# Optimization experiments

Measured on AMD Instinct MI355X. Metric: run time of the kernel, lower is better.

The kernel has to match this reference:

```python
import jax, jax.numpy as jnp
import numpy as np

ALPHA = 0.4
STEPS = 4
EPSILON = 0.005

N_NODES = 4096
N_EDGES = 131072
D_FEAT = 128


def setup_inputs() -> dict:
    key = jax.random.key(0)
    k1, k2, k3, k4 = jax.random.split(key, 4)
    x = jax.random.normal(k1, (N_NODES, D_FEAT), dtype=jnp.float32)
    src = jax.random.randint(k2, (N_EDGES,), 0, N_NODES)
    dst = jax.random.randint(k3, (N_EDGES,), 0, N_NODES)
    edge_index = jnp.stack([src, dst], axis=0).astype(jnp.int64)
    edge_attr = jax.random.uniform(k4, (N_EDGES,), dtype=jnp.float32)
    return {"x": x, "edge_index": edge_index, "edge_attr": edge_attr}


def reference(x, edge_index, edge_attr):
    # PPR power series: result = sum_i theta_i * A_i, where
    #   A_0 = edge pattern with unit values, A_1 = A (edge_attr),
    #   A_{i+1} = threshold_eps(A @ A_i).
    # Dense [N,N] representation: thresholding (dropping entries < eps in the
    # sparse original) is exactly zeroing those entries here; jit-compatible
    # since sparse nnz is data-dependent.
    N = x.shape[0]
    src, dst = edge_index[0], edge_index[1]
    A = jnp.zeros((N, N), dtype=edge_attr.dtype).at[src, dst].add(edge_attr)
    P0 = jnp.zeros((N, N), dtype=edge_attr.dtype).at[src, dst].add(1.0)

    mats = [P0, A]
    for _ in range(1, STEPS - 1):
        M = A @ mats[-1]
        M = jnp.where(M >= EPSILON, M, jnp.zeros((), dtype=M.dtype))
        mats.append(M)

    thetas = [ALPHA * (1.0 - ALPHA) ** i for i in range(STEPS)]
    out = thetas[0] * mats[0]
    for t, m in zip(thetas[1:], mats[1:]):
        out = out + t * m
    return out
```

## Files before the change

### kernel.cpp

```cpp
#include <hip/hip_runtime.h>

#define N_NODES 4096
#define EPS 0.005f
#define TH0 0.4f
#define TH1 0.24f
#define TH2 0.144f
#define TH3 0.0864f
#define JTILE 512
#define NTILES (N_NODES / JTILE)
#define RCAP 80
#define CPAD 16

typedef float v4f __attribute__((ext_vector_type(4)));
typedef unsigned int u32x4 __attribute__((ext_vector_type(4)));


static __device__ __forceinline__ float lo16(unsigned int u) {
    return __uint_as_float(u << 16);
}
static __device__ __forceinline__ float hi16(unsigned int u) {
    return __uint_as_float(u & 0xffff0000u);
}

static __device__ __forceinline__ unsigned short f2bf(float f) {
    union { float f; unsigned int i; } x;
    x.f = f;
    unsigned int r = x.i + 0x7fff + ((x.i >> 16) & 1u);
    return (unsigned short)(r >> 16);
}

__global__ void scatter_kernel(const int* __restrict__ idx,
                               const float* __restrict__ attr, int E,
                               int* __restrict__ counts, int2* __restrict__ pairs) {
    int e = blockIdx.x * blockDim.x + threadIdx.x;
    if (e < E) {
        int s = idx[e];
        int d = idx[e + E];
        float a = attr[e];
        int pos = atomicAdd(&counts[s * CPAD], 1);
        if (pos < RCAP) pairs[s * RCAP + pos] = make_int2(d, __float_as_int(a));
    }
}

__global__ __launch_bounds__(256)
void m2_kernel(const int* __restrict__ counts, const int2* __restrict__ pairs,
               unsigned short* __restrict__ m2) {
    __shared__ float acc[N_NODES];
    __shared__ int   kcol[RCAP];
    __shared__ float kval[RCAP];
    __shared__ int   kcnt[RCAP];
    int i = blockIdx.x;
    int t = threadIdx.x;
    float4 z = make_float4(0.f, 0.f, 0.f, 0.f);
    for (int j4 = t; j4 < N_NODES / 4; j4 += 256) ((float4*)acc)[j4] = z;
    int cnt = min(counts[i * CPAD], RCAP);
    if (t < cnt) {
        int2 p = pairs[i * RCAP + t];
        kcol[t] = p.x;
        kval[t] = __int_as_float(p.y);
        kcnt[t] = min(counts[p.x * CPAD], RCAP);
    }
    __syncthreads();
    int gid = t >> 3, gl = t & 7;
    for (int q = gid; q < cnt; q += 32) {
        float a = kval[q];
        int fb = kcol[q] * RCAP;
        int fn = kcnt[q];
        for (int f = gl; f < fn; f += 8) {
            int2 p = pairs[fb + f];
            unsafeAtomicAdd(&acc[p.x], a * __int_as_float(p.y));
        }
    }
    __syncthreads();
    size_t rb = (size_t)i * N_NODES;
    for (int j4 = t; j4 < N_NODES / 4; j4 += 256) {
        float4 v = ((const float4*)acc)[j4];
        ushort4 r;
        r.x = (v.x >= EPS) ? f2bf(v.x) : (unsigned short)0;
        r.y = (v.y >= EPS) ? f2bf(v.y) : (unsigned short)0;
        r.z = (v.z >= EPS) ? f2bf(v.z) : (unsigned short)0;
        r.w = (v.w >= EPS) ? f2bf(v.w) : (unsigned short)0;
        ((ushort4*)(m2 + rb))[j4] = r;
    }
}

__global__ __launch_bounds__(128)
void out_kernel(const int* __restrict__ counts, const int2* __restrict__ pairs,
                const unsigned short* __restrict__ m2,
                float* __restrict__ out) {
    __shared__ float ap[2][JTILE];
    int lin = blockIdx.x;
    int tile = lin & 7;
    int jb = tile * JTILE;
    int t = threadIdx.x;
    int w = t >> 6, lane = t & 63;
    int i = 2 * (lin >> 3) + w;
    float* apw = ap[w];
    ((float4*)apw)[lane] = make_float4(0.f, 0.f, 0.f, 0.f);
    ((float4*)apw)[64 + lane] = make_float4(0.f, 0.f, 0.f, 0.f);
    int cnt = min(counts[i * CPAD], RCAP);
    const int2* pi = pairs + i * RCAP;
    for (int e = lane; e < cnt; e += 64) {
        int2 p = pi[e];
        int cl = p.x - jb;
        if ((unsigned)cl < (unsigned)JTILE)
            unsafeAtomicAdd(&apw[cl], TH0 + TH1 * __int_as_float(p.y));
    }
    int cnt8 = (cnt + 7) & ~7;
    const unsigned short* m2l = m2 + jb + 8 * lane;
    v4f acc0 = 0.f, acc1 = 0.f;
    for (int e = 0; e < cnt8; e += 8) {
        int4 q01 = *(const int4*)(pi + e);
        int4 q23 = *(const int4*)(pi + e + 2);
        int4 q45 = *(const int4*)(pi + e + 4);
        int4 q67 = *(const int4*)(pi + e + 6);
        int k0 = __builtin_amdgcn_readfirstlane(q01.x);
        int k1 = __builtin_amdgcn_readfirstlane(q01.z);
        int k2 = __builtin_amdgcn_readfirstlane(q23.x);
        int k3 = __builtin_amdgcn_readfirstlane(q23.z);
        int k4 = __builtin_amdgcn_readfirstlane(q45.x);
        int k5 = __builtin_amdgcn_readfirstlane(q45.z);
        int k6 = __builtin_amdgcn_readfirstlane(q67.x);
        int k7 = __builtin_amdgcn_readfirstlane(q67.z);
        float a0 = __int_as_float(q01.y), a1 = __int_as_float(q01.w);
        float a2 = __int_as_float(q23.y), a3 = __int_as_float(q23.w);
        float a4 = __int_as_float(q45.y), a5 = __int_as_float(q45.w);
        float a6 = __int_as_float(q67.y), a7 = __int_as_float(q67.w);
        u32x4 u0 = *(const u32x4*)(m2l + (size_t)k0 * N_NODES);
        u32x4 u1 = *(const u32x4*)(m2l + (size_t)k1 * N_NODES);
        u32x4 u2 = *(const u32x4*)(m2l + (size_t)k2 * N_NODES);
        u32x4 u3 = *(const u32x4*)(m2l + (size_t)k3 * N_NODES);
        u32x4 u4 = *(const u32x4*)(m2l + (size_t)k4 * N_NODES);
        u32x4 u5 = *(const u32x4*)(m2l + (size_t)k5 * N_NODES);
        u32x4 u6 = *(const u32x4*)(m2l + (size_t)k6 * N_NODES);
        u32x4 u7 = *(const u32x4*)(m2l + (size_t)k7 * N_NODES);
#define ACC8(uu, aa)                                \
        acc0.x = fmaf(aa, lo16(uu.x), acc0.x);      \
        acc0.y = fmaf(aa, hi16(uu.x), acc0.y);      \
        acc0.z = fmaf(aa, lo16(uu.y), acc0.z);      \
        acc0.w = fmaf(aa, hi16(uu.y), acc0.w);      \
        acc1.x = fmaf(aa, lo16(uu.z), acc1.x);      \
        acc1.y = fmaf(aa, hi16(uu.z), acc1.y);      \
        acc1.z = fmaf(aa, lo16(uu.w), acc1.z);      \
        acc1.w = fmaf(aa, hi16(uu.w), acc1.w);
        ACC8(u0, a0) ACC8(u1, a1) ACC8(u2, a2) ACC8(u3, a3)
        ACC8(u4, a4) ACC8(u5, a5) ACC8(u6, a6) ACC8(u7, a7)
#undef ACC8
    }
    u32x4 um = *(const u32x4*)(m2 + (size_t)i * N_NODES + jb + 8 * lane);
    float4 p0 = ((const float4*)apw)[2 * lane];
    float4 p1 = ((const float4*)apw)[2 * lane + 1];
    v4f r0, r1;
    r0.x = p0.x + TH2 * lo16(um.x) + TH3 * ((acc0.x >= EPS) ? acc0.x : 0.0f);
    r0.y = p0.y + TH2 * hi16(um.x) + TH3 * ((acc0.y >= EPS) ? acc0.y : 0.0f);
    r0.z = p0.z + TH2 * lo16(um.y) + TH3 * ((acc0.z >= EPS) ? acc0.z : 0.0f);
    r0.w = p0.w + TH2 * hi16(um.y) + TH3 * ((acc0.w >= EPS) ? acc0.w : 0.0f);
    r1.x = p1.x + TH2 * lo16(um.z) + TH3 * ((acc1.x >= EPS) ? acc1.x : 0.0f);
    r1.y = p1.y + TH2 * hi16(um.z) + TH3 * ((acc1.y >= EPS) ? acc1.y : 0.0f);
    r1.z = p1.z + TH2 * lo16(um.w) + TH3 * ((acc1.z >= EPS) ? acc1.z : 0.0f);
    r1.w = p1.w + TH2 * hi16(um.w) + TH3 * ((acc1.w >= EPS) ? acc1.w : 0.0f);
    float* o = out + (size_t)i * N_NODES + jb + 8 * lane;
    __builtin_nontemporal_store(r0, (v4f*)o);
    __builtin_nontemporal_store(r1, (v4f*)(o + 4));
}

extern "C" void kernel_launch(void* const* d_in, const int* in_sizes, int n_in,
                              void* d_out, int out_size, void* d_ws, size_t ws_size,
                              hipStream_t stream) {
    const int* idx = (const int*)d_in[1];
    const float* attr = (const float*)d_in[2];
    int E = in_sizes[1] / 2;

    char* ws = (char*)d_ws;
    int*  counts = (int*)(ws);
    int2* pairs  = (int2*)(ws + (256 << 10));
    unsigned short* m2 = (unsigned short*)(ws + (4 << 20));
    float* out   = (float*)d_out;

    (void)hipMemsetAsync(ws, 0,
                         (256 << 10) + N_NODES * RCAP * sizeof(int2), stream);
    scatter_kernel<<<(E + 255) / 256, 256, 0, stream>>>(idx, attr, E, counts, pairs);
    m2_kernel<<<N_NODES, 256, 0, stream>>>(counts, pairs, m2);
    out_kernel<<<(N_NODES / 2) * NTILES, 128, 0, stream>>>(counts, pairs, m2, out);
}
```

Before: 179.3 us.

## Software-pipeline gather loads in out_kernel and unroll m2 atomic scatter loop

Restructures the out_kernel neighbor loop into a double-buffered pipeline. The next batch of eight m2 row loads is issued before the current batch is consumed, and pair indices are prefetched two batches ahead. The diagonal m2 load is hoisted to the start and launch bounds now request 3 blocks per SM. In m2_kernel each lane issues four pair loads before its atomics, giving more memory-level parallelism. The costs are much higher register pressure, which could force spills under the tighter launch bound, and more complex loop control.

```diff
diff --git a/kernel.cpp b/kernel.cpp
--- a/kernel.cpp
+++ b/kernel.cpp
@@ -62,13 +62,21 @@
     }
     __syncthreads();
     int gid = t >> 3, gl = t & 7;
+    int2 zp = make_int2(0, 0);
     for (int q = gid; q < cnt; q += 32) {
         float a = kval[q];
         int fb = kcol[q] * RCAP;
         int fn = kcnt[q];
-        for (int f = gl; f < fn; f += 8) {
-            int2 p = pairs[fb + f];
-            unsafeAtomicAdd(&acc[p.x], a * __int_as_float(p.y));
+        for (int f0 = gl; f0 < fn; f0 += 32) {
+            int i1 = f0 + 8, i2 = f0 + 16, i3 = f0 + 24;
+            int2 p0 = pairs[fb + f0];
+            int2 p1 = (i1 < fn) ? pairs[fb + i1] : zp;
+            int2 p2 = (i2 < fn) ? pairs[fb + i2] : zp;
+            int2 p3 = (i3 < fn) ? pairs[fb + i3] : zp;
+            unsafeAtomicAdd(&acc[p0.x], a * __int_as_float(p0.y));
+            unsafeAtomicAdd(&acc[p1.x], a * __int_as_float(p1.y));
+            unsafeAtomicAdd(&acc[p2.x], a * __int_as_float(p2.y));
+            unsafeAtomicAdd(&acc[p3.x], a * __int_as_float(p3.y));
         }
     }
     __syncthreads();
@@ -84,7 +92,41 @@
     }
 }
 
-__global__ __launch_bounds__(128)
+#define ACC8(uu, aa)                                \
+        acc0.x = fmaf(aa, lo16(uu.x), acc0.x);      \
+        acc0.y = fmaf(aa, hi16(uu.x), acc0.y);      \
+        acc0.z = fmaf(aa, lo16(uu.y), acc0.z);      \
+        acc0.w = fmaf(aa, hi16(uu.y), acc0.w);      \
+        acc1.x = fmaf(aa, lo16(uu.z), acc1.x);      \
+        acc1.y = fmaf(aa, hi16(uu.z), acc1.y);      \
+        acc1.z = fmaf(aa, lo16(uu.w), acc1.z);      \
+        acc1.w = fmaf(aa, hi16(uu.w), acc1.w);
+
+#define EXTR(E0_, E1_, E2_, E3_, K, A)                                              \
+        K##0 = __builtin_amdgcn_readfirstlane(E0_.x); A##0 = __int_as_float(E0_.y); \
+        K##1 = __builtin_amdgcn_readfirstlane(E0_.z); A##1 = __int_as_float(E0_.w); \
+        K##2 = __builtin_amdgcn_readfirstlane(E1_.x); A##2 = __int_as_float(E1_.y); \
+        K##3 = __builtin_amdgcn_readfirstlane(E1_.z); A##3 = __int_as_float(E1_.w); \
+        K##4 = __builtin_amdgcn_readfirstlane(E2_.x); A##4 = __int_as_float(E2_.y); \
+        K##5 = __builtin_amdgcn_readfirstlane(E2_.z); A##5 = __int_as_float(E2_.w); \
+        K##6 = __builtin_amdgcn_readfirstlane(E3_.x); A##6 = __int_as_float(E3_.y); \
+        K##7 = __builtin_amdgcn_readfirstlane(E3_.z); A##7 = __int_as_float(E3_.w);
+
+#define ISSUE8(K, U)                                                    \
+        U##0 = *(const u32x4*)(m2l + (size_t)K##0 * N_NODES);           \
+        U##1 = *(const u32x4*)(m2l + (size_t)K##1 * N_NODES);           \
+        U##2 = *(const u32x4*)(m2l + (size_t)K##2 * N_NODES);           \
+        U##3 = *(const u32x4*)(m2l + (size_t)K##3 * N_NODES);           \
+        U##4 = *(const u32x4*)(m2l + (size_t)K##4 * N_NODES);           \
+        U##5 = *(const u32x4*)(m2l + (size_t)K##5 * N_NODES);           \
+        U##6 = *(const u32x4*)(m2l + (size_t)K##6 * N_NODES);           \
+        U##7 = *(const u32x4*)(m2l + (size_t)K##7 * N_NODES);
+
+#define CONSUME8(U, A)                                                      \
+        ACC8(U##0, A##0) ACC8(U##1, A##1) ACC8(U##2, A##2) ACC8(U##3, A##3) \
+        ACC8(U##4, A##4) ACC8(U##5, A##5) ACC8(U##6, A##6) ACC8(U##7, A##7)
+
+__global__ __launch_bounds__(128, 3)
 void out_kernel(const int* __restrict__ counts, const int2* __restrict__ pairs,
                 const unsigned short* __restrict__ m2,
                 float* __restrict__ out) {
@@ -96,8 +138,10 @@
     int w = t >> 6, lane = t & 63;
     int i = 2 * (lin >> 3) + w;
     float* apw = ap[w];
-    ((float4*)apw)[lane] = make_float4(0.f, 0.f, 0.f, 0.f);
-    ((float4*)apw)[64 + lane] = make_float4(0.f, 0.f, 0.f, 0.f);
+    u32x4 um = *(const u32x4*)(m2 + (size_t)i * N_NODES + jb + 8 * lane);
+    float4 z4 = make_float4(0.f, 0.f, 0.f, 0.f);
+    ((float4*)apw)[lane] = z4;
+    ((float4*)apw)[64 + lane] = z4;
     int cnt = min(counts[i * CPAD], RCAP);
     const int2* pi = pairs + i * RCAP;
     for (int e = lane; e < cnt; e += 64) {
@@ -109,45 +153,44 @@
     int cnt8 = (cnt + 7) & ~7;
     const unsigned short* m2l = m2 + jb + 8 * lane;
     v4f acc0 = 0.f, acc1 = 0.f;
-    for (int e = 0; e < cnt8; e += 8) {
-        int4 q01 = *(const int4*)(pi + e);
-        int4 q23 = *(const int4*)(pi + e + 2);
-        int4 q45 = *(const int4*)(pi + e + 4);
-        int4 q67 = *(const int4*)(pi + e + 6);
-        int k0 = __builtin_amdgcn_readfirstlane(q01.x);
-        int k1 = __builtin_amdgcn_readfirstlane(q01.z);
-        int k2 = __builtin_amdgcn_readfirstlane(q23.x);
-        int k3 = __builtin_amdgcn_readfirstlane(q23.z);
-        int k4 = __builtin_amdgcn_readfirstlane(q45.x);
-        int k5 = __builtin_amdgcn_readfirstlane(q45.z);
-        int k6 = __builtin_amdgcn_readfirstlane(q67.x);
-        int k7 = __builtin_amdgcn_readfirstlane(q67.z);
-        float a0 = __int_as_float(q01.y), a1 = __int_as_float(q01.w);
-        float a2 = __int_as_float(q23.y), a3 = __int_as_float(q23.w);
-        float a4 = __int_as_float(q45.y), a5 = __int_as_float(q45.w);
-        float a6 = __int_as_float(q67.y), a7 = __int_as_float(q67.w);
-        u32x4 u0 = *(const u32x4*)(m2l + (size_t)k0 * N_NODES);
-        u32x4 u1 = *(const u32x4*)(m2l + (size_t)k1 * N_NODES);
-        u32x4 u2 = *(const u32x4*)(m2l + (size_t)k2 * N_NODES);
-        u32x4 u3 = *(const u32x4*)(m2l + (size_t)k3 * N_NODES);
-        u32x4 u4 = *(const u32x4*)(m2l + (size_t)k4 * N_NODES);
-        u32x4 u5 = *(const u32x4*)(m2l + (size_t)k5 * N_NODES);
-        u32x4 u6 = *(const u32x4*)(m2l + (size_t)k6 * N_NODES);
-        u32x4 u7 = *(const u32x4*)(m2l + (size_t)k7 * N_NODES);
-#define ACC8(uu, aa)                                \
-        acc0.x = fmaf(aa, lo16(uu.x), acc0.x);      \
-        acc0.y = fmaf(aa, hi16(uu.x), acc0.y);      \
-        acc0.z = fmaf(aa, lo16(uu.y), acc0.z);      \
-        acc0.w = fmaf(aa, hi16(uu.y), acc0.w);      \
-        acc1.x = fmaf(aa, lo16(uu.z), acc1.x);      \
-        acc1.y = fmaf(aa, hi16(uu.z), acc1.y);      \
-        acc1.z = fmaf(aa, lo16(uu.w), acc1.z);      \
-        acc1.w = fmaf(aa, hi16(uu.w), acc1.w);
-        ACC8(u0, a0) ACC8(u1, a1) ACC8(u2, a2) ACC8(u3, a3)
-        ACC8(u4, a4) ACC8(u5, a5) ACC8(u6, a6) ACC8(u7, a7)
-#undef ACC8
-    }
-    u32x4 um = *(const u32x4*)(m2 + (size_t)i * N_NODES + jb + 8 * lane);
+    const int4* pi4 = (const int4*)pi;
+
+    if (cnt8 > 0) {
+        int4 eA0, eA1, eA2, eA3, eB0, eB1, eB2, eB3;
+        int kA0, kA1, kA2, kA3, kA4, kA5, kA6, kA7;
+        int kB0, kB1, kB2, kB3, kB4, kB5, kB6, kB7;
+        float aA0, aA1, aA2, aA3, aA4, aA5, aA6, aA7;
+        float aB0, aB1, aB2, aB3, aB4, aB5, aB6, aB7;
+        u32x4 uA0, uA1, uA2, uA3, uA4, uA5, uA6, uA7;
+        u32x4 uB0, uB1, uB2, uB3, uB4, uB5, uB6, uB7;
+
+        eA0 = pi4[0]; eA1 = pi4[1]; eA2 = pi4[2]; eA3 = pi4[3];
+        int b1 = (cnt8 > 8) ? 4 : 0;
+        eB0 = pi4[b1]; eB1 = pi4[b1 + 1]; eB2 = pi4[b1 + 2]; eB3 = pi4[b1 + 3];
+        EXTR(eA0, eA1, eA2, eA3, kA, aA)
+        ISSUE8(kA, uA)
+
+        int e = 0;
+        for (;;) {
+            if (e + 8 < cnt8) {
+                EXTR(eB0, eB1, eB2, eB3, kB, aB)
+                int nb = min(e + 16, cnt8 - 8) >> 1;
+                eA0 = pi4[nb]; eA1 = pi4[nb + 1]; eA2 = pi4[nb + 2]; eA3 = pi4[nb + 3];
+                ISSUE8(kB, uB)
+            }
+            CONSUME8(uA, aA)
+            e += 8; if (e >= cnt8) break;
+            if (e + 8 < cnt8) {
+                EXTR(eA0, eA1, eA2, eA3, kA, aA)
+                int nb = min(e + 16, cnt8 - 8) >> 1;
+                eB0 = pi4[nb]; eB1 = pi4[nb + 1]; eB2 = pi4[nb + 2]; eB3 = pi4[nb + 3];
+                ISSUE8(kA, uA)
+            }
+            CONSUME8(uB, aB)
+            e += 8; if (e >= cnt8) break;
+        }
+    }
+
     float4 p0 = ((const float4*)apw)[2 * lane];
     float4 p1 = ((const float4*)apw)[2 * lane + 1];
     v4f r0, r1;
```

Result: slower. 248.0 us (+38.3%).

## Halve output column tile and unroll neighbor atomic accumulation in m2 kernel

Applied to the files above, without the earlier changes.

The output kernel now processes 256-column tiles with four columns per lane, doubling the grid and halving per-thread accumulators and loads. Block index decoding is remapped so the extra tiles come from the high bits of the block id. The m2 kernel's inner scatter loop is unrolled by four, with guarded loads to expose more memory-level parallelism. In exchange, each row's pair list is re-read for twice as many tiles, and the padded iterations issue zero-valued atomics.

```diff
diff --git a/kernel.cpp b/kernel.cpp
--- a/kernel.cpp
+++ b/kernel.cpp
@@ -6,13 +6,13 @@
 #define TH1 0.24f
 #define TH2 0.144f
 #define TH3 0.0864f
-#define JTILE 512
+#define JTILE 256
 #define NTILES (N_NODES / JTILE)
 #define RCAP 80
 #define CPAD 16
 
 typedef float v4f __attribute__((ext_vector_type(4)));
-typedef unsigned int u32x4 __attribute__((ext_vector_type(4)));
+typedef unsigned int u32x2 __attribute__((ext_vector_type(2)));
 
 
 static __device__ __forceinline__ float lo16(unsigned int u) {
@@ -62,13 +62,21 @@
     }
     __syncthreads();
     int gid = t >> 3, gl = t & 7;
+    int2 zp = make_int2(0, 0);
     for (int q = gid; q < cnt; q += 32) {
         float a = kval[q];
         int fb = kcol[q] * RCAP;
         int fn = kcnt[q];
-        for (int f = gl; f < fn; f += 8) {
-            int2 p = pairs[fb + f];
-            unsafeAtomicAdd(&acc[p.x], a * __int_as_float(p.y));
+        for (int f0 = gl; f0 < fn; f0 += 32) {
+            int i1 = f0 + 8, i2 = f0 + 16, i3 = f0 + 24;
+            int2 p0 = pairs[fb + f0];
+            int2 p1 = (i1 < fn) ? pairs[fb + i1] : zp;
+            int2 p2 = (i2 < fn) ? pairs[fb + i2] : zp;
+            int2 p3 = (i3 < fn) ? pairs[fb + i3] : zp;
+            unsafeAtomicAdd(&acc[p0.x], a * __int_as_float(p0.y));
+            unsafeAtomicAdd(&acc[p1.x], a * __int_as_float(p1.y));
+            unsafeAtomicAdd(&acc[p2.x], a * __int_as_float(p2.y));
+            unsafeAtomicAdd(&acc[p3.x], a * __int_as_float(p3.y));
         }
     }
     __syncthreads();
@@ -90,14 +98,13 @@
                 float* __restrict__ out) {
     __shared__ float ap[2][JTILE];
     int lin = blockIdx.x;
-    int tile = lin & 7;
+    int tile = (lin & 7) | ((lin >> 14) << 3);
     int jb = tile * JTILE;
     int t = threadIdx.x;
     int w = t >> 6, lane = t & 63;
-    int i = 2 * (lin >> 3) + w;
+    int i = 2 * ((lin >> 3) & 2047) + w;
     float* apw = ap[w];
     ((float4*)apw)[lane] = make_float4(0.f, 0.f, 0.f, 0.f);
-    ((float4*)apw)[64 + lane] = make_float4(0.f, 0.f, 0.f, 0.f);
     int cnt = min(counts[i * CPAD], RCAP);
     const int2* pi = pairs + i * RCAP;
     for (int e = lane; e < cnt; e += 64) {
@@ -107,8 +114,8 @@
             unsafeAtomicAdd(&apw[cl], TH0 + TH1 * __int_as_float(p.y));
     }
     int cnt8 = (cnt + 7) & ~7;
-    const unsigned short* m2l = m2 + jb + 8 * lane;
-    v4f acc0 = 0.f, acc1 = 0.f;
+    const unsigned short* m2l = m2 + jb + 4 * lane;
+    v4f acc0 = 0.f;
     for (int e = 0; e < cnt8; e += 8) {
         int4 q01 = *(const int4*)(pi + e);
         int4 q23 = *(const int4*)(pi + e + 2);
@@ -126,42 +133,32 @@
         float a2 = __int_as_float(q23.y), a3 = __int_as_float(q23.w);
         float a4 = __int_as_float(q45.y), a5 = __int_as_float(q45.w);
         float a6 = __int_as_float(q67.y), a7 = __int_as_float(q67.w);
-        u32x4 u0 = *(const u32x4*)(m2l + (size_t)k0 * N_NODES);
-        u32x4 u1 = *(const u32x4*)(m2l + (size_t)k1 * N_NODES);
-        u32x4 u2 = *(const u32x4*)(m2l + (size_t)k2 * N_NODES);
-        u32x4 u3 = *(const u32x4*)(m2l + (size_t)k3 * N_NODES);
-        u32x4 u4 = *(const u32x4*)(m2l + (size_t)k4 * N_NODES);
-        u32x4 u5 = *(const u32x4*)(m2l + (size_t)k5 * N_NODES);
-        u32x4 u6 = *(const u32x4*)(m2l + (size_t)k6 * N_NODES);
-        u32x4 u7 = *(const u32x4*)(m2l + (size_t)k7 * N_NODES);
-#define ACC8(uu, aa)                                \
+        u32x2 u0 = *(const u32x2*)(m2l + (size_t)k0 * N_NODES);
+        u32x2 u1 = *(const u32x2*)(m2l + (size_t)k1 * N_NODES);
+        u32x2 u2 = *(const u32x2*)(m2l + (size_t)k2 * N_NODES);
+        u32x2 u3 = *(const u32x2*)(m2l + (size_t)k3 * N_NODES);
+        u32x2 u4 = *(const u32x2*)(m2l + (size_t)k4 * N_NODES);
+        u32x2 u5 = *(const u32x2*)(m2l + (size_t)k5 * N_NODES);
+        u32x2 u6 = *(const u32x2*)(m2l + (size_t)k6 * N_NODES);
+        u32x2 u7 = *(const u32x2*)(m2l + (size_t)k7 * N_NODES);
+#define ACC4(uu, aa)                                \
         acc0.x = fmaf(aa, lo16(uu.x), acc0.x);      \
         acc0.y = fmaf(aa, hi16(uu.x), acc0.y);      \
         acc0.z = fmaf(aa, lo16(uu.y), acc0.z);      \
-        acc0.w = fmaf(aa, hi16(uu.y), acc0.w);      \
-        acc1.x = fmaf(aa, lo16(uu.z), acc1.x);      \
-        acc1.y = fmaf(aa, hi16(uu.z), acc1.y);      \
-        acc1.z = fmaf(aa, lo16(uu.w), acc1.z);      \
-        acc1.w = fmaf(aa, hi16(uu.w), acc1.w);
-        ACC8(u0, a0) ACC8(u1, a1) ACC8(u2, a2) ACC8(u3, a3)
-        ACC8(u4, a4) ACC8(u5, a5) ACC8(u6, a6) ACC8(u7, a7)
-#undef ACC8
+        acc0.w = fmaf(aa, hi16(uu.y), acc0.w);
+        ACC4(u0, a0) ACC4(u1, a1) ACC4(u2, a2) ACC4(u3, a3)
+        ACC4(u4, a4) ACC4(u5, a5) ACC4(u6, a6) ACC4(u7, a7)
+#undef ACC4
     }
-    u32x4 um = *(const u32x4*)(m2 + (size_t)i * N_NODES + jb + 8 * lane);
-    float4 p0 = ((const float4*)apw)[2 * lane];
-    float4 p1 = ((const float4*)apw)[2 * lane + 1];
-    v4f r0, r1;
+    u32x2 um = *(const u32x2*)(m2 + (size_t)i * N_NODES + jb + 4 * lane);
+    float4 p0 = ((const float4*)apw)[lane];
+    v4f r0;
     r0.x = p0.x + TH2 * lo16(um.x) + TH3 * ((acc0.x >= EPS) ? acc0.x : 0.0f);
     r0.y = p0.y + TH2 * hi16(um.x) + TH3 * ((acc0.y >= EPS) ? acc0.y : 0.0f);
     r0.z = p0.z + TH2 * lo16(um.y) + TH3 * ((acc0.z >= EPS) ? acc0.z : 0.0f);
     r0.w = p0.w + TH2 * hi16(um.y) + TH3 * ((acc0.w >= EPS) ? acc0.w : 0.0f);
-    r1.x = p1.x + TH2 * lo16(um.z) + TH3 * ((acc1.x >= EPS) ? acc1.x : 0.0f);
-    r1.y = p1.y + TH2 * hi16(um.z) + TH3 * ((acc1.y >= EPS) ? acc1.y : 0.0f);
-    r1.z = p1.z + TH2 * lo16(um.w) + TH3 * ((acc1.z >= EPS) ? acc1.z : 0.0f);
-    r1.w = p1.w + TH2 * hi16(um.w) + TH3 * ((acc1.w >= EPS) ? acc1.w : 0.0f);
-    float* o = out + (size_t)i * N_NODES + jb + 8 * lane;
+    float* o = out + (size_t)i * N_NODES + jb + 4 * lane;
     __builtin_nontemporal_store(r0, (v4f*)o);
-    __builtin_nontemporal_store(r1, (v4f*)(o + 4));
 }
 
 extern "C" void kernel_launch(void* const* d_in, const int* in_sizes, int n_in,
```

Measured after the change: 225.2 us. 1.26x slower.

## Store M2 as fp16 and accumulate with v_fma_mix; unroll m2 scatter loop

Applied to the files above, without the earlier changes.

Changes the intermediate M2 matrix from bf16 to fp16 so the out kernel can use v_fma_mix_f32 inline asm, which converts each fp16 operand inside the FMA and drops the separate shift and mask extraction instructions. The m2 kernel's inner scatter loop is also unrolled four-way so more pair loads are in flight before the LDS atomics issue. fp16 gives more mantissa bits but less range than bf16; the values here are small positive sums above eps, so they should fit. Inline asm limits how freely the compiler can schedule the loop.

```diff
diff --git a/kernel.cpp b/kernel.cpp
--- a/kernel.cpp
+++ b/kernel.cpp
@@ -1,4 +1,5 @@
 #include <hip/hip_runtime.h>
+#include <hip/hip_fp16.h>
 
 #define N_NODES 4096
 #define EPS 0.005f
@@ -15,18 +16,8 @@
 typedef unsigned int u32x4 __attribute__((ext_vector_type(4)));
 
 
-static __device__ __forceinline__ float lo16(unsigned int u) {
-    return __uint_as_float(u << 16);
-}
-static __device__ __forceinline__ float hi16(unsigned int u) {
-    return __uint_as_float(u & 0xffff0000u);
-}
-
-static __device__ __forceinline__ unsigned short f2bf(float f) {
-    union { float f; unsigned int i; } x;
-    x.f = f;
-    unsigned int r = x.i + 0x7fff + ((x.i >> 16) & 1u);
-    return (unsigned short)(r >> 16);
+static __device__ __forceinline__ unsigned short f2h(float f) {
+    return __half_as_ushort(__float2half(f));
 }
 
 __global__ void scatter_kernel(const int* __restrict__ idx,
@@ -62,13 +53,21 @@
     }
     __syncthreads();
     int gid = t >> 3, gl = t & 7;
+    int2 zp = make_int2(0, 0);
     for (int q = gid; q < cnt; q += 32) {
         float a = kval[q];
         int fb = kcol[q] * RCAP;
         int fn = kcnt[q];
-        for (int f = gl; f < fn; f += 8) {
-            int2 p = pairs[fb + f];
-            unsafeAtomicAdd(&acc[p.x], a * __int_as_float(p.y));
+        for (int f0 = gl; f0 < fn; f0 += 32) {
+            int i1 = f0 + 8, i2 = f0 + 16, i3 = f0 + 24;
+            int2 p0 = pairs[fb + f0];
+            int2 p1 = (i1 < fn) ? pairs[fb + i1] : zp;
+            int2 p2 = (i2 < fn) ? pairs[fb + i2] : zp;
+            int2 p3 = (i3 < fn) ? pairs[fb + i3] : zp;
+            unsafeAtomicAdd(&acc[p0.x], a * __int_as_float(p0.y));
+            unsafeAtomicAdd(&acc[p1.x], a * __int_as_float(p1.y));
+            unsafeAtomicAdd(&acc[p2.x], a * __int_as_float(p2.y));
+            unsafeAtomicAdd(&acc[p3.x], a * __int_as_float(p3.y));
         }
     }
     __syncthreads();
@@ -76,13 +75,23 @@
     for (int j4 = t; j4 < N_NODES / 4; j4 += 256) {
         float4 v = ((const float4*)acc)[j4];
         ushort4 r;
-        r.x = (v.x >= EPS) ? f2bf(v.x) : (unsigned short)0;
-        r.y = (v.y >= EPS) ? f2bf(v.y) : (unsigned short)0;
-        r.z = (v.z >= EPS) ? f2bf(v.z) : (unsigned short)0;
-        r.w = (v.w >= EPS) ? f2bf(v.w) : (unsigned short)0;
+        r.x = (v.x >= EPS) ? f2h(v.x) : (unsigned short)0;
+        r.y = (v.y >= EPS) ? f2h(v.y) : (unsigned short)0;
+        r.z = (v.z >= EPS) ? f2h(v.z) : (unsigned short)0;
+        r.w = (v.w >= EPS) ? f2h(v.w) : (unsigned short)0;
         ((ushort4*)(m2 + rb))[j4] = r;
     }
 }
+
+#define MIX2(uu_word, aclo, achi, aa)                                          \
+    asm("v_fma_mix_f32 %0, %1, %2, %0 op_sel_hi:[0,1,0]"                       \
+        : "+v"(aclo) : "v"(aa), "v"(uu_word));                                 \
+    asm("v_fma_mix_f32 %0, %1, %2, %0 op_sel:[0,1,0] op_sel_hi:[0,1,0]"        \
+        : "+v"(achi) : "v"(aa), "v"(uu_word));
+
+#define MIX8(uu, aa)                                                           \
+    MIX2(uu.x, ac0, ac1, aa) MIX2(uu.y, ac2, ac3, aa)                          \
+    MIX2(uu.z, ac4, ac5, aa) MIX2(uu.w, ac6, ac7, aa)
 
 __global__ __launch_bounds__(128)
 void out_kernel(const int* __restrict__ counts, const int2* __restrict__ pairs,
@@ -108,7 +117,8 @@
     }
     int cnt8 = (cnt + 7) & ~7;
     const unsigned short* m2l = m2 + jb + 8 * lane;
-    v4f acc0 = 0.f, acc1 = 0.f;
+    float ac0 = 0.f, ac1 = 0.f, ac2 = 0.f, ac3 = 0.f;
+    float ac4 = 0.f, ac5 = 0.f, ac6 = 0.f, ac7 = 0.f;
     for (int e = 0; e < cnt8; e += 8) {
         int4 q01 = *(const int4*)(pi + e);
         int4 q23 = *(const int4*)(pi + e + 2);
@@ -134,31 +144,24 @@
         u32x4 u5 = *(const u32x4*)(m2l + (size_t)k5 * N_NODES);
         u32x4 u6 = *(const u32x4*)(m2l + (size_t)k6 * N_NODES);
         u32x4 u7 = *(const u32x4*)(m2l + (size_t)k7 * N_NODES);
-#define ACC8(uu, aa)                                \
-        acc0.x = fmaf(aa, lo16(uu.x), acc0.x);      \
-        acc0.y = fmaf(aa, hi16(uu.x), acc0.y);      \
-        acc0.z = fmaf(aa, lo16(uu.y), acc0.z);      \
-        acc0.w = fmaf(aa, hi16(uu.y), acc0.w);      \
-        acc1.x = fmaf(aa, lo16(uu.z), acc1.x);      \
-        acc1.y = fmaf(aa, hi16(uu.z), acc1.y);      \
-        acc1.z = fmaf(aa, lo16(uu.w), acc1.z);      \
-        acc1.w = fmaf(aa, hi16(uu.w), acc1.w);
-        ACC8(u0, a0) ACC8(u1, a1) ACC8(u2, a2) ACC8(u3, a3)
-        ACC8(u4, a4) ACC8(u5, a5) ACC8(u6, a6) ACC8(u7, a7)
-#undef ACC8
+        MIX8(u0, a0) MIX8(u1, a1) MIX8(u2, a2) MIX8(u3, a3)
+        MIX8(u4, a4) MIX8(u5, a5) MIX8(u6, a6) MIX8(u7, a7)
     }
     u32x4 um = *(const u32x4*)(m2 + (size_t)i * N_NODES + jb + 8 * lane);
+    unsigned ux = um.x, uy = um.y, uz = um.z, uw = um.w;
+    __half2 hx = *(__half2*)&ux, hy = *(__half2*)&uy;
+    __half2 hz = *(__half2*)&uz, hw = *(__half2*)&uw;
     float4 p0 = ((const float4*)apw)[2 * lane];
     float4 p1 = ((const float4*)apw)[2 * lane + 1];
     v4f r0, r1;
-    r0.x = p0.x + TH2 * lo16(um.x) + TH3 * ((acc0.x >= EPS) ? acc0.x : 0.0f);
-    r0.y = p0.y + TH2 * hi16(um.x) + TH3 * ((acc0.y >= EPS) ? acc0.y : 0.0f);
-    r0.z = p0.z + TH2 * lo16(um.y) + TH3 * ((acc0.z >= EPS) ? acc0.z : 0.0f);
-    r0.w = p0.w + TH2 * hi16(um.y) + TH3 * ((acc0.w >= EPS) ? acc0.w : 0.0f);
-    r1.x = p1.x + TH2 * lo16(um.z) + TH3 * ((acc1.x >= EPS) ? acc1.x : 0.0f);
-    r1.y = p1.y + TH2 * hi16(um.z) + TH3 * ((acc1.y >= EPS) ? acc1.y : 0.0f);
-    r1.z = p1.z + TH2 * lo16(um.w) + TH3 * ((acc1.z >= EPS) ? acc1.z : 0.0f);
-    r1.w = p1.w + TH2 * hi16(um.w) + TH3 * ((acc1.w >= EPS) ? acc1.w : 0.0f);
+    r0.x = p0.x + TH2 * __low2float(hx)  + TH3 * ((ac0 >= EPS) ? ac0 : 0.0f);
+    r0.y = p0.y + TH2 * __high2float(hx) + TH3 * ((ac1 >= EPS) ? ac1 : 0.0f);
+    r0.z = p0.z + TH2 * __low2float(hy)  + TH3 * ((ac2 >= EPS) ? ac2 : 0.0f);
+    r0.w = p0.w + TH2 * __high2float(hy) + TH3 * ((ac3 >= EPS) ? ac3 : 0.0f);
+    r1.x = p1.x + TH2 * __low2float(hz)  + TH3 * ((ac4 >= EPS) ? ac4 : 0.0f);
+    r1.y = p1.y + TH2 * __high2float(hz) + TH3 * ((ac5 >= EPS) ? ac5 : 0.0f);
+    r1.z = p1.z + TH2 * __low2float(hw)  + TH3 * ((ac6 >= EPS) ? ac6 : 0.0f);
+    r1.w = p1.w + TH2 * __high2float(hw) + TH3 * ((ac7 >= EPS) ? ac7 : 0.0f);
     float* o = out + (size_t)i * N_NODES + jb + 8 * lane;
     __builtin_nontemporal_store(r0, (v4f*)o);
     __builtin_nontemporal_store(r1, (v4f*)(o + 4));
```

Measured after the change: 187.2 us. 4.4% more time.
